# Kernel optimization log

Measured on AMD Instinct MI355X. Metric: run time of the kernel, lower is better.

Reference implementation:

```python
import jax, jax.numpy as jnp
import numpy as np

N_VEH = 40000
N_PATH = 400000
N_ACTOR = 128
N_MAP = 128
ACT_C = 32
PAT_C = 32
SIZE = N_ACTOR + N_MAP + ACT_C + PAT_C  # 320
HID = SIZE // 2  # 160
EPS = 1e-5


def _gn1(x, w, b):
    # GroupNorm with 1 group over channel dim of [N, C]: per-row normalize, per-channel affine
    mu = jnp.mean(x, axis=-1, keepdims=True)
    var = jnp.mean(jnp.square(x - mu), axis=-1, keepdims=True)
    return (x - mu) * jax.lax.rsqrt(var + EPS) * w + b


def setup_inputs() -> dict:
    key = jax.random.key(0)
    ks = jax.random.split(key, 12)
    inp = {
        "actors": jax.random.normal(ks[0], (N_VEH, N_ACTOR), jnp.float32),
        "paths": jax.random.normal(ks[1], (N_PATH, N_MAP), jnp.float32),
        "Z_act": jax.random.normal(ks[2], (N_VEH, ACT_C), jnp.float32),
        "Z_pat": jax.random.normal(ks[3], (N_PATH, PAT_C), jnp.float32),
        "u": jax.random.randint(ks[4], (N_PATH,), 0, N_VEH, jnp.int64 if jax.config.jax_enable_x64 else jnp.int32),
        # LinRes params (LaneGCN LinearRes: Linear(bias=False) -> GN -> ReLU -> Linear(bias=False) -> GN -> +transform(x) -> ReLU)
        "w1": jax.random.normal(ks[5], (HID, SIZE), jnp.float32) / np.sqrt(SIZE),
        "w2": jax.random.normal(ks[6], (HID, HID), jnp.float32) / np.sqrt(HID),
        "wt": jax.random.normal(ks[7], (HID, SIZE), jnp.float32) / np.sqrt(SIZE),
        "g1w": jnp.ones((HID,), jnp.float32),
        "g1b": jnp.zeros((HID,), jnp.float32),
        "g2w": jnp.ones((HID,), jnp.float32),
        "g2b": jnp.zeros((HID,), jnp.float32),
        # final head Linear(HID, 1)
        "wh": jax.random.normal(ks[8], (1, HID), jnp.float32) / np.sqrt(HID),
        "bh": jnp.zeros((1,), jnp.float32),
    }
    return inp


def reference(actors, paths, Z_act, Z_pat, u, w1, w2, wt, g1w, g1b, g2w, g2b, wh, bh):
    # edge-indexed gather + concat: [N_PATH, SIZE]
    x = jnp.concatenate([paths, Z_pat, actors[u], Z_act[u]], axis=-1)
    h = jnp.einsum('ns,hs->nh', x, w1)
    h = jax.nn.relu(_gn1(h, g1w, g1b))
    h = jnp.einsum('nh,gh->ng', h, w2)
    h = _gn1(h, g2w, g2b)
    h = jax.nn.relu(h + jnp.einsum('ns,hs->nh', x, wt))
    logits = jnp.einsum('nh,oh->no', h, wh) + bh
    return logits
```

## Files before the change

### kernel.cpp

```cpp
#include <hip/hip_runtime.h>
#include <hip/hip_bf16.h>

typedef short short8 __attribute__((ext_vector_type(8)));
typedef float floatx4 __attribute__((ext_vector_type(4)));

#define XP 328
#define HP 168

__device__ __forceinline__ unsigned short f2bf(float f) {
    __hip_bfloat16 h = __float2bfloat16(f);
    return __builtin_bit_cast(unsigned short, h);
}
__device__ __forceinline__ float bf2f(unsigned short s) {
    __hip_bfloat16 h = __builtin_bit_cast(__hip_bfloat16, s);
    return __bfloat162float(h);
}

__global__ void pack_wc(const float* __restrict__ w1, const float* __restrict__ wt,
                        unsigned short* __restrict__ dst) {
    int i = blockIdx.x * 256 + threadIdx.x;
    if (i >= 320 * 320) return;
    int j = i & 7;
    int lane = (i >> 3) & 63;
    int r = i >> 9;
    int kb = r % 10;
    int t = r / 10;
    int n = t * 16 + (lane & 15);
    int k = kb * 32 + ((lane >> 4) << 3) + j;
    float v = (n < 160) ? w1[n * 320 + k] : wt[(n - 160) * 320 + k];
    dst[i] = f2bf(v);
}

__global__ void pack_w2(const float* __restrict__ w2, unsigned short* __restrict__ dst) {
    int i = blockIdx.x * 256 + threadIdx.x;
    if (i >= 160 * 160) return;
    int j = i & 7;
    int lane = (i >> 3) & 63;
    int r = i >> 9;
    int kb = r % 5;
    int t = r / 5;
    int n = t * 16 + (lane & 15);
    int k = kb * 32 + ((lane >> 4) << 3) + j;
    dst[i] = f2bf(w2[n * 160 + k]);
}

__global__ __launch_bounds__(256, 3) void fused_kernel(
    const float* __restrict__ actors, const float* __restrict__ paths,
    const float* __restrict__ Z_act, const float* __restrict__ Z_pat,
    const int* __restrict__ u,
    const unsigned short* __restrict__ pB1, const unsigned short* __restrict__ pB2,
    const float* __restrict__ g1w, const float* __restrict__ g1b,
    const float* __restrict__ g2w, const float* __restrict__ g2b,
    const float* __restrict__ wh, const float* __restrict__ bh,
    float* __restrict__ out)
{
    __shared__ __align__(16) char smem[43520];
    unsigned short* lX  = (unsigned short*)smem;
    unsigned short* lH1 = (unsigned short*)smem;
    unsigned short* lHT = (unsigned short*)(smem + 21504);
    float* sSum  = (float*)(smem + 41984);
    float* sSq   = sSum + 128;
    float* sMu   = sSum + 256;
    float* sRstd = sSum + 320;

    const int tid  = threadIdx.x;
    const int wave = tid >> 6;
    const int lane = tid & 63;
    const int quad = lane >> 4;
    const int l15  = lane & 15;
    const int row0 = blockIdx.x * 64;

    float4 vD[10], vG[10];
    int uv[10];
    #pragma unroll
    for (int i = 0; i < 10; i++) {
        int f = i * 256 + tid;
        int r = f / 40, q = f - r * 40;
        const float* src = (q < 32) ? (paths + (size_t)(row0 + r) * 128 + q * 4)
                                    : (Z_pat + (size_t)(row0 + r) * 32 + (q - 32) * 4);
        vD[i] = *(const float4*)src;
        uv[i] = u[row0 + r];
    }
    #pragma unroll
    for (int i = 0; i < 10; i++) {
        int f = i * 256 + tid;
        int r = f / 40, q = f - r * 40;
        (void)r;
        int un = uv[i];
        const float* src = (q < 32) ? (actors + (size_t)un * 128 + q * 4)
                                    : (Z_act + (size_t)un * 32 + (q - 32) * 4);
        vG[i] = *(const float4*)src;
    }
    #pragma unroll
    for (int i = 0; i < 10; i++) {
        int f = i * 256 + tid;
        int r = f / 40, q = f - r * 40;
        ushort4 sv;
        sv.x = f2bf(vD[i].x); sv.y = f2bf(vD[i].y); sv.z = f2bf(vD[i].z); sv.w = f2bf(vD[i].w);
        *(ushort4*)(lX + r * XP + q * 4) = sv;
    }
    #pragma unroll
    for (int i = 0; i < 10; i++) {
        int f = i * 256 + tid;
        int r = f / 40, q = f - r * 40;
        ushort4 sv;
        sv.x = f2bf(vG[i].x); sv.y = f2bf(vG[i].y); sv.z = f2bf(vG[i].z); sv.w = f2bf(vG[i].w);
        *(ushort4*)(lX + r * XP + 160 + q * 4) = sv;
    }

    short8 bA[5], bB[5];
    #pragma unroll
    for (int ti = 0; ti < 5; ti++) {
        int t = wave * 5 + ti;
        bA[ti] = *(const short8*)(pB1 + ((size_t)(t * 10 + 0) * 64 + lane) * 8);
        bB[ti] = *(const short8*)(pB1 + ((size_t)(t * 10 + 1) * 64 + lane) * 8);
    }
    __syncthreads();

    floatx4 fzero = {0.f, 0.f, 0.f, 0.f};
    floatx4 acc[4][5];
    #pragma unroll
    for (int i = 0; i < 4; i++)
        #pragma unroll
        for (int j = 0; j < 5; j++) acc[i][j] = fzero;

    #pragma unroll
    for (int kb = 0; kb < 10; kb++) {
        short8 a[4];
        #pragma unroll
        for (int mt = 0; mt < 4; mt++)
            a[mt] = *(const short8*)(lX + (mt * 16 + l15) * XP + kb * 32 + quad * 8);
        short8 bN[5];
        if (kb + 2 < 10) {
            #pragma unroll
            for (int ti = 0; ti < 5; ti++) {
                int t = wave * 5 + ti;
                bN[ti] = *(const short8*)(pB1 + ((size_t)(t * 10 + kb + 2) * 64 + lane) * 8);
            }
        }
        #pragma unroll
        for (int ti = 0; ti < 5; ti++) {
            #pragma unroll
            for (int mt = 0; mt < 4; mt++)
                acc[mt][ti] = __builtin_amdgcn_mfma_f32_16x16x32_bf16(a[mt], bA[ti], acc[mt][ti], 0, 0, 0);
        }
        #pragma unroll
        for (int ti = 0; ti < 5; ti++) { bA[ti] = bB[ti]; bB[ti] = bN[ti]; }
    }
    __syncthreads();

    if (wave >= 2) {
        int wn = wave - 2;
        #pragma unroll
        for (int mtp = 0; mtp < 4; mtp++)
            #pragma unroll
            for (int ti = 0; ti < 5; ti++)
                #pragma unroll
                for (int r = 0; r < 4; r++)
                    lHT[((((wn * 4 + mtp) * 5 + ti) * 4 + r) << 6) + lane] = f2bf(acc[mtp][ti][r]);
    } else {
        float s[16], q2[16];
        #pragma unroll
        for (int mt = 0; mt < 4; mt++)
            #pragma unroll
            for (int r = 0; r < 4; r++) {
                float sv = 0.f, qv = 0.f;
                #pragma unroll
                for (int ti = 0; ti < 5; ti++) {
                    float v = acc[mt][ti][r];
                    sv += v; qv += v * v;
                }
                s[mt * 4 + r] = sv; q2[mt * 4 + r] = qv;
            }
        #pragma unroll
        for (int off = 1; off <= 8; off <<= 1)
            #pragma unroll
            for (int k = 0; k < 16; k++) {
                s[k]  += __shfl_xor(s[k],  off, 64);
                q2[k] += __shfl_xor(q2[k], off, 64);
            }
        if (l15 == 0) {
            #pragma unroll
            for (int mt = 0; mt < 4; mt++)
                #pragma unroll
                for (int r = 0; r < 4; r++) {
                    int m = mt * 16 + quad * 4 + r;
                    sSum[wave * 64 + m] = s[mt * 4 + r];
                    sSq[wave * 64 + m]  = q2[mt * 4 + r];
                }
        }
    }
    __syncthreads();

    if (tid < 64) {
        float ts = sSum[tid] + sSum[64 + tid];
        float tq = sSq[tid] + sSq[64 + tid];
        float mu = ts * (1.f / 160.f);
        float var = tq * (1.f / 160.f) - mu * mu;
        sMu[tid] = mu;
        sRstd[tid] = rsqrtf(var + 1e-5f);
    }
    __syncthreads();

    if (wave < 2) {
        float gw[5], gb[5];
        #pragma unroll
        for (int ti = 0; ti < 5; ti++) {
            int n = wave * 80 + ti * 16 + l15;
            gw[ti] = g1w[n]; gb[ti] = g1b[n];
        }
        #pragma unroll
        for (int mt = 0; mt < 4; mt++)
            #pragma unroll
            for (int r = 0; r < 4; r++) {
                int m = mt * 16 + quad * 4 + r;
                float mu = sMu[m], rs = sRstd[m];
                #pragma unroll
                for (int ti = 0; ti < 5; ti++) {
                    float v = (acc[mt][ti][r] - mu) * rs * gw[ti] + gb[ti];
                    v = fmaxf(v, 0.f);
                    lH1[m * HP + wave * 80 + ti * 16 + l15] = f2bf(v);
                }
            }
    }

    const int wm = wave & 1, wn = wave >> 1;
    short8 b2A[5], b2B[5];
    #pragma unroll
    for (int ti = 0; ti < 5; ti++) {
        int t = wn * 5 + ti;
        b2A[ti] = *(const short8*)(pB2 + ((size_t)(t * 5 + 0) * 64 + lane) * 8);
        b2B[ti] = *(const short8*)(pB2 + ((size_t)(t * 5 + 1) * 64 + lane) * 8);
    }
    __syncthreads();

    floatx4 acc2[2][5];
    #pragma unroll
    for (int i = 0; i < 2; i++)
        #pragma unroll
        for (int j = 0; j < 5; j++) acc2[i][j] = fzero;

    #pragma unroll
    for (int kb = 0; kb < 5; kb++) {
        short8 a[2];
        #pragma unroll
        for (int mt = 0; mt < 2; mt++)
            a[mt] = *(const short8*)(lH1 + (wm * 32 + mt * 16 + l15) * HP + kb * 32 + quad * 8);
        short8 bN[5];
        if (kb + 2 < 5) {
            #pragma unroll
            for (int ti = 0; ti < 5; ti++) {
                int t = wn * 5 + ti;
                bN[ti] = *(const short8*)(pB2 + ((size_t)(t * 5 + kb + 2) * 64 + lane) * 8);
            }
        }
        #pragma unroll
        for (int ti = 0; ti < 5; ti++) {
            #pragma unroll
            for (int mt = 0; mt < 2; mt++)
                acc2[mt][ti] = __builtin_amdgcn_mfma_f32_16x16x32_bf16(a[mt], b2A[ti], acc2[mt][ti], 0, 0, 0);
        }
        #pragma unroll
        for (int ti = 0; ti < 5; ti++) { b2A[ti] = b2B[ti]; b2B[ti] = bN[ti]; }
    }

    {
        float s[8], q2[8];
        #pragma unroll
        for (int mt = 0; mt < 2; mt++)
            #pragma unroll
            for (int r = 0; r < 4; r++) {
                float sv = 0.f, qv = 0.f;
                #pragma unroll
                for (int ti = 0; ti < 5; ti++) {
                    float v = acc2[mt][ti][r];
                    sv += v; qv += v * v;
                }
                s[mt * 4 + r] = sv; q2[mt * 4 + r] = qv;
            }
        #pragma unroll
        for (int off = 1; off <= 8; off <<= 1)
            #pragma unroll
            for (int k = 0; k < 8; k++) {
                s[k]  += __shfl_xor(s[k],  off, 64);
                q2[k] += __shfl_xor(q2[k], off, 64);
            }
        if (l15 == 0) {
            #pragma unroll
            for (int mt = 0; mt < 2; mt++)
                #pragma unroll
                for (int r = 0; r < 4; r++) {
                    int m = wm * 32 + mt * 16 + quad * 4 + r;
                    sSum[wn * 64 + m] = s[mt * 4 + r];
                    sSq[wn * 64 + m]  = q2[mt * 4 + r];
                }
        }
    }
    __syncthreads();

    if (tid < 64) {
        float ts = sSum[tid] + sSum[64 + tid];
        float tq = sSq[tid] + sSq[64 + tid];
        float mu = ts * (1.f / 160.f);
        float var = tq * (1.f / 160.f) - mu * mu;
        sMu[tid] = mu;
        sRstd[tid] = rsqrtf(var + 1e-5f);
    }
    __syncthreads();

    {
        float g2wv[5], g2bv[5], whv[5];
        #pragma unroll
        for (int ti = 0; ti < 5; ti++) {
            int n = wn * 80 + ti * 16 + l15;
            g2wv[ti] = g2w[n]; g2bv[ti] = g2b[n]; whv[ti] = wh[n];
        }
        float dp[8];
        #pragma unroll
        for (int k = 0; k < 8; k++) dp[k] = 0.f;
        #pragma unroll
        for (int mt = 0; mt < 2; mt++)
            #pragma unroll
            for (int r = 0; r < 4; r++) {
                int m = wm * 32 + mt * 16 + quad * 4 + r;
                float mu = sMu[m], rs = sRstd[m];
                #pragma unroll
                for (int ti = 0; ti < 5; ti++) {
                    float v = (acc2[mt][ti][r] - mu) * rs * g2wv[ti] + g2bv[ti];
                    v += bf2f(lHT[((((wn * 4 + (wm * 2 + mt)) * 5 + ti) * 4 + r) << 6) + lane]);
                    v = fmaxf(v, 0.f);
                    dp[mt * 4 + r] += v * whv[ti];
                }
            }
        #pragma unroll
        for (int off = 1; off <= 8; off <<= 1)
            #pragma unroll
            for (int k = 0; k < 8; k++) dp[k] += __shfl_xor(dp[k], off, 64);
        __syncthreads();
        if (l15 == 0) {
            #pragma unroll
            for (int mt = 0; mt < 2; mt++)
                #pragma unroll
                for (int r = 0; r < 4; r++) {
                    int m = wm * 32 + mt * 16 + quad * 4 + r;
                    sSum[wn * 64 + m] = dp[mt * 4 + r];
                }
        }
    }
    __syncthreads();
    if (tid < 64) out[row0 + tid] = sSum[tid] + sSum[64 + tid] + bh[0];
}

extern "C" void kernel_launch(void* const* d_in, const int* in_sizes, int n_in,
                              void* d_out, int out_size, void* d_ws, size_t ws_size,
                              hipStream_t stream) {
    const float* actors = (const float*)d_in[0];
    const float* paths  = (const float*)d_in[1];
    const float* Z_act  = (const float*)d_in[2];
    const float* Z_pat  = (const float*)d_in[3];
    const int*   u      = (const int*)d_in[4];
    const float* w1     = (const float*)d_in[5];
    const float* w2     = (const float*)d_in[6];
    const float* wt     = (const float*)d_in[7];
    const float* g1w    = (const float*)d_in[8];
    const float* g1b    = (const float*)d_in[9];
    const float* g2w    = (const float*)d_in[10];
    const float* g2b    = (const float*)d_in[11];
    const float* wh     = (const float*)d_in[12];
    const float* bh     = (const float*)d_in[13];
    float* out = (float*)d_out;

    unsigned short* pB1 = (unsigned short*)d_ws;
    unsigned short* pB2 = pB1 + 320 * 320;

    hipLaunchKernelGGL(pack_wc, dim3(400), dim3(256), 0, stream, w1, wt, pB1);
    hipLaunchKernelGGL(pack_w2, dim3(100), dim3(256), 0, stream, w2, pB2);
    hipLaunchKernelGGL(fused_kernel, dim3(400000 / 64), dim3(256), 0, stream,
                       actors, paths, Z_act, Z_pat, u, pB1, pB2,
                       g1w, g1b, g2w, g2b, wh, bh, out);
}
```

Baseline: 500.2 us.

## Shrink blocks to 32 rows and two waves, remove cross-wave GroupNorm reductions

The fused kernel now processes 32 rows per block with 128 threads, so each wave owns full 160-wide output rows in GEMM1 (wave 0 the main branch, wave 1 the transform branch) and 16 full rows in GEMM2. Row statistics for both GroupNorms are computed in-wave via shuffles, which removes the shared sSum/sSq exchange buffers and several __syncthreads barriers, and halves LDS per block. B-fragment prefetch depth goes from two steps to one with more tiles per wave. The trade-off is more blocks, higher per-thread register pressure (20 accumulators, 10-entry B buffers), and a GEMM1 split where wave 0 also does the GN1 epilogue while wave 1 only stores, so the work is imbalanced.

```diff
diff --git a/kernel.cpp b/kernel.cpp
--- a/kernel.cpp
+++ b/kernel.cpp
@@ -44,7 +44,7 @@
     dst[i] = f2bf(w2[n * 160 + k]);
 }
 
-__global__ __launch_bounds__(256, 3) void fused_kernel(
+__global__ __launch_bounds__(128, 3) void fused_kernel(
     const float* __restrict__ actors, const float* __restrict__ paths,
     const float* __restrict__ Z_act, const float* __restrict__ Z_pat,
     const int* __restrict__ u,
@@ -54,27 +54,23 @@
     const float* __restrict__ wh, const float* __restrict__ bh,
     float* __restrict__ out)
 {
-    __shared__ __align__(16) char smem[43520];
+    __shared__ __align__(16) char smem[21504];
     unsigned short* lX  = (unsigned short*)smem;
     unsigned short* lH1 = (unsigned short*)smem;
-    unsigned short* lHT = (unsigned short*)(smem + 21504);
-    float* sSum  = (float*)(smem + 41984);
-    float* sSq   = sSum + 128;
-    float* sMu   = sSum + 256;
-    float* sRstd = sSum + 320;
+    unsigned short* lHT = (unsigned short*)(smem + 10752);
 
     const int tid  = threadIdx.x;
     const int wave = tid >> 6;
     const int lane = tid & 63;
     const int quad = lane >> 4;
     const int l15  = lane & 15;
-    const int row0 = blockIdx.x * 64;
+    const int row0 = blockIdx.x * 32;
 
     float4 vD[10], vG[10];
     int uv[10];
     #pragma unroll
     for (int i = 0; i < 10; i++) {
-        int f = i * 256 + tid;
+        int f = i * 128 + tid;
         int r = f / 40, q = f - r * 40;
         const float* src = (q < 32) ? (paths + (size_t)(row0 + r) * 128 + q * 4)
                                     : (Z_pat + (size_t)(row0 + r) * 32 + (q - 32) * 4);
@@ -83,9 +79,8 @@
     }
     #pragma unroll
     for (int i = 0; i < 10; i++) {
-        int f = i * 256 + tid;
-        int r = f / 40, q = f - r * 40;
-        (void)r;
+        int f = i * 128 + tid;
+        int q = f % 40;
         int un = uv[i];
         const float* src = (q < 32) ? (actors + (size_t)un * 128 + q * 4)
                                     : (Z_act + (size_t)un * 32 + (q - 32) * 4);
@@ -93,7 +88,7 @@
     }
     #pragma unroll
     for (int i = 0; i < 10; i++) {
-        int f = i * 256 + tid;
+        int f = i * 128 + tid;
         int r = f / 40, q = f - r * 40;
         ushort4 sv;
         sv.x = f2bf(vD[i].x); sv.y = f2bf(vD[i].y); sv.z = f2bf(vD[i].z); sv.w = f2bf(vD[i].w);
@@ -101,72 +96,60 @@
     }
     #pragma unroll
     for (int i = 0; i < 10; i++) {
-        int f = i * 256 + tid;
+        int f = i * 128 + tid;
         int r = f / 40, q = f - r * 40;
         ushort4 sv;
         sv.x = f2bf(vG[i].x); sv.y = f2bf(vG[i].y); sv.z = f2bf(vG[i].z); sv.w = f2bf(vG[i].w);
         *(ushort4*)(lX + r * XP + 160 + q * 4) = sv;
     }
 
-    short8 bA[5], bB[5];
-    #pragma unroll
-    for (int ti = 0; ti < 5; ti++) {
-        int t = wave * 5 + ti;
-        bA[ti] = *(const short8*)(pB1 + ((size_t)(t * 10 + 0) * 64 + lane) * 8);
-        bB[ti] = *(const short8*)(pB1 + ((size_t)(t * 10 + 1) * 64 + lane) * 8);
+    short8 bC[10], bN[10];
+    #pragma unroll
+    for (int ti = 0; ti < 10; ti++) {
+        int t = wave * 10 + ti;
+        bC[ti] = *(const short8*)(pB1 + ((size_t)(t * 10 + 0) * 64 + lane) * 8);
     }
     __syncthreads();
 
     floatx4 fzero = {0.f, 0.f, 0.f, 0.f};
-    floatx4 acc[4][5];
-    #pragma unroll
-    for (int i = 0; i < 4; i++)
-        #pragma unroll
-        for (int j = 0; j < 5; j++) acc[i][j] = fzero;
+    floatx4 acc[2][10];
+    #pragma unroll
+    for (int i = 0; i < 2; i++)
+        #pragma unroll
+        for (int j = 0; j < 10; j++) acc[i][j] = fzero;
 
     #pragma unroll
     for (int kb = 0; kb < 10; kb++) {
-        short8 a[4];
-        #pragma unroll
-        for (int mt = 0; mt < 4; mt++)
+        short8 a[2];
+        #pragma unroll
+        for (int mt = 0; mt < 2; mt++)
             a[mt] = *(const short8*)(lX + (mt * 16 + l15) * XP + kb * 32 + quad * 8);
-        short8 bN[5];
-        if (kb + 2 < 10) {
-            #pragma unroll
-            for (int ti = 0; ti < 5; ti++) {
-                int t = wave * 5 + ti;
-                bN[ti] = *(const short8*)(pB1 + ((size_t)(t * 10 + kb + 2) * 64 + lane) * 8);
-            }
-        }
-        #pragma unroll
-        for (int ti = 0; ti < 5; ti++) {
-            #pragma unroll
-            for (int mt = 0; mt < 4; mt++)
-                acc[mt][ti] = __builtin_amdgcn_mfma_f32_16x16x32_bf16(a[mt], bA[ti], acc[mt][ti], 0, 0, 0);
-        }
-        #pragma unroll
-        for (int ti = 0; ti < 5; ti++) { bA[ti] = bB[ti]; bB[ti] = bN[ti]; }
+        if (kb < 9) {
+            #pragma unroll
+            for (int ti = 0; ti < 10; ti++) {
+                int t = wave * 10 + ti;
+                bN[ti] = *(const short8*)(pB1 + ((size_t)(t * 10 + kb + 1) * 64 + lane) * 8);
+            }
+        }
+        #pragma unroll
+        for (int ti = 0; ti < 10; ti++)
+            #pragma unroll
+            for (int mt = 0; mt < 2; mt++)
+                acc[mt][ti] = __builtin_amdgcn_mfma_f32_16x16x32_bf16(a[mt], bC[ti], acc[mt][ti], 0, 0, 0);
+        #pragma unroll
+        for (int ti = 0; ti < 10; ti++) bC[ti] = bN[ti];
     }
     __syncthreads();
 
-    if (wave >= 2) {
-        int wn = wave - 2;
-        #pragma unroll
-        for (int mtp = 0; mtp < 4; mtp++)
-            #pragma unroll
-            for (int ti = 0; ti < 5; ti++)
-                #pragma unroll
-                for (int r = 0; r < 4; r++)
-                    lHT[((((wn * 4 + mtp) * 5 + ti) * 4 + r) << 6) + lane] = f2bf(acc[mtp][ti][r]);
-    } else {
-        float s[16], q2[16];
-        #pragma unroll
-        for (int mt = 0; mt < 4; mt++)
+    if (wave == 0) {
+        float s[8], q2[8];
+        #pragma unroll
+        for (int mt = 0; mt < 2; mt++)
             #pragma unroll
             for (int r = 0; r < 4; r++) {
                 float sv = 0.f, qv = 0.f;
                 #pragma unroll
-                for (int ti = 0; ti < 5; ti++) {
+                for (int ti = 0; ti < 10; ti++) {
                     float v = acc[mt][ti][r];
                     sv += v; qv += v * v;
                 }
@@ -175,180 +158,121 @@
         #pragma unroll
         for (int off = 1; off <= 8; off <<= 1)
             #pragma unroll
-            for (int k = 0; k < 16; k++) {
+            for (int k = 0; k < 8; k++) {
                 s[k]  += __shfl_xor(s[k],  off, 64);
                 q2[k] += __shfl_xor(q2[k], off, 64);
             }
-        if (l15 == 0) {
-            #pragma unroll
-            for (int mt = 0; mt < 4; mt++)
+        float gw[10], gb[10];
+        #pragma unroll
+        for (int ti = 0; ti < 10; ti++) {
+            int n = ti * 16 + l15;
+            gw[ti] = g1w[n]; gb[ti] = g1b[n];
+        }
+        #pragma unroll
+        for (int mt = 0; mt < 2; mt++)
+            #pragma unroll
+            for (int r = 0; r < 4; r++) {
+                float mu = s[mt * 4 + r] * (1.f / 160.f);
+                float var = q2[mt * 4 + r] * (1.f / 160.f) - mu * mu;
+                float rs = rsqrtf(var + 1e-5f);
+                int m = mt * 16 + quad * 4 + r;
+                #pragma unroll
+                for (int ti = 0; ti < 10; ti++) {
+                    float v = (acc[mt][ti][r] - mu) * rs * gw[ti] + gb[ti];
+                    v = fmaxf(v, 0.f);
+                    lH1[m * HP + ti * 16 + l15] = f2bf(v);
+                }
+            }
+    } else {
+        #pragma unroll
+        for (int mt = 0; mt < 2; mt++)
+            #pragma unroll
+            for (int ti = 0; ti < 10; ti++)
                 #pragma unroll
                 for (int r = 0; r < 4; r++) {
                     int m = mt * 16 + quad * 4 + r;
-                    sSum[wave * 64 + m] = s[mt * 4 + r];
-                    sSq[wave * 64 + m]  = q2[mt * 4 + r];
+                    lHT[m * HP + ti * 16 + l15] = f2bf(acc[mt][ti][r]);
                 }
-        }
-    }
+    }
+
+    short8 b2C[10], b2N[10];
+    #pragma unroll
+    for (int ti = 0; ti < 10; ti++)
+        b2C[ti] = *(const short8*)(pB2 + ((size_t)(ti * 5 + 0) * 64 + lane) * 8);
     __syncthreads();
 
-    if (tid < 64) {
-        float ts = sSum[tid] + sSum[64 + tid];
-        float tq = sSq[tid] + sSq[64 + tid];
-        float mu = ts * (1.f / 160.f);
-        float var = tq * (1.f / 160.f) - mu * mu;
-        sMu[tid] = mu;
-        sRstd[tid] = rsqrtf(var + 1e-5f);
-    }
-    __syncthreads();
-
-    if (wave < 2) {
-        float gw[5], gb[5];
-        #pragma unroll
-        for (int ti = 0; ti < 5; ti++) {
-            int n = wave * 80 + ti * 16 + l15;
-            gw[ti] = g1w[n]; gb[ti] = g1b[n];
-        }
-        #pragma unroll
-        for (int mt = 0; mt < 4; mt++)
+    floatx4 acc2[10];
+    #pragma unroll
+    for (int j = 0; j < 10; j++) acc2[j] = fzero;
+
+    #pragma unroll
+    for (int kb = 0; kb < 5; kb++) {
+        short8 a = *(const short8*)(lH1 + (wave * 16 + l15) * HP + kb * 32 + quad * 8);
+        if (kb < 4) {
+            #pragma unroll
+            for (int ti = 0; ti < 10; ti++)
+                b2N[ti] = *(const short8*)(pB2 + ((size_t)(ti * 5 + kb + 1) * 64 + lane) * 8);
+        }
+        #pragma unroll
+        for (int ti = 0; ti < 10; ti++)
+            acc2[ti] = __builtin_amdgcn_mfma_f32_16x16x32_bf16(a, b2C[ti], acc2[ti], 0, 0, 0);
+        #pragma unroll
+        for (int ti = 0; ti < 10; ti++) b2C[ti] = b2N[ti];
+    }
+
+    {
+        float s[4], q2[4];
+        #pragma unroll
+        for (int r = 0; r < 4; r++) {
+            float sv = 0.f, qv = 0.f;
+            #pragma unroll
+            for (int ti = 0; ti < 10; ti++) {
+                float v = acc2[ti][r];
+                sv += v; qv += v * v;
+            }
+            s[r] = sv; q2[r] = qv;
+        }
+        #pragma unroll
+        for (int off = 1; off <= 8; off <<= 1)
             #pragma unroll
             for (int r = 0; r < 4; r++) {
-                int m = mt * 16 + quad * 4 + r;
-                float mu = sMu[m], rs = sRstd[m];
-                #pragma unroll
-                for (int ti = 0; ti < 5; ti++) {
-                    float v = (acc[mt][ti][r] - mu) * rs * gw[ti] + gb[ti];
-                    v = fmaxf(v, 0.f);
-                    lH1[m * HP + wave * 80 + ti * 16 + l15] = f2bf(v);
-                }
-            }
-    }
-
-    const int wm = wave & 1, wn = wave >> 1;
-    short8 b2A[5], b2B[5];
-    #pragma unroll
-    for (int ti = 0; ti < 5; ti++) {
-        int t = wn * 5 + ti;
-        b2A[ti] = *(const short8*)(pB2 + ((size_t)(t * 5 + 0) * 64 + lane) * 8);
-        b2B[ti] = *(const short8*)(pB2 + ((size_t)(t * 5 + 1) * 64 + lane) * 8);
-    }
-    __syncthreads();
-
-    floatx4 acc2[2][5];
-    #pragma unroll
-    for (int i = 0; i < 2; i++)
-        #pragma unroll
-        for (int j = 0; j < 5; j++) acc2[i][j] = fzero;
-
-    #pragma unroll
-    for (int kb = 0; kb < 5; kb++) {
-        short8 a[2];
-        #pragma unroll
-        for (int mt = 0; mt < 2; mt++)
-            a[mt] = *(const short8*)(lH1 + (wm * 32 + mt * 16 + l15) * HP + kb * 32 + quad * 8);
-        short8 bN[5];
-        if (kb + 2 < 5) {
-            #pragma unroll
-            for (int ti = 0; ti < 5; ti++) {
-                int t = wn * 5 + ti;
-                bN[ti] = *(const short8*)(pB2 + ((size_t)(t * 5 + kb + 2) * 64 + lane) * 8);
-            }
-        }
-        #pragma unroll
-        for (int ti = 0; ti < 5; ti++) {
-            #pragma unroll
-            for (int mt = 0; mt < 2; mt++)
-                acc2[mt][ti] = __builtin_amdgcn_mfma_f32_16x16x32_bf16(a[mt], b2A[ti], acc2[mt][ti], 0, 0, 0);
-        }
-        #pragma unroll
-        for (int ti = 0; ti < 5; ti++) { b2A[ti] = b2B[ti]; b2B[ti] = bN[ti]; }
-    }
-
-    {
-        float s[8], q2[8];
-        #pragma unroll
-        for (int mt = 0; mt < 2; mt++)
-            #pragma unroll
-            for (int r = 0; r < 4; r++) {
-                float sv = 0.f, qv = 0.f;
-                #pragma unroll
-                for (int ti = 0; ti < 5; ti++) {
-                    float v = acc2[mt][ti][r];
-                    sv += v; qv += v * v;
-                }
-                s[mt * 4 + r] = sv; q2[mt * 4 + r] = qv;
-            }
+                s[r]  += __shfl_xor(s[r],  off, 64);
+                q2[r] += __shfl_xor(q2[r], off, 64);
+            }
+        float g2wv[10], g2bv[10], whv[10];
+        #pragma unroll
+        for (int ti = 0; ti < 10; ti++) {
+            int n = ti * 16 + l15;
+            g2wv[ti] = g2w[n]; g2bv[ti] = g2b[n]; whv[ti] = wh[n];
+        }
+        float dp[4];
+        #pragma unroll
+        for (int r = 0; r < 4; r++) {
+            float mu = s[r] * (1.f / 160.f);
+            float var = q2[r] * (1.f / 160.f) - mu * mu;
+            float rs = rsqrtf(var + 1e-5f);
+            int m = wave * 16 + quad * 4 + r;
+            float d = 0.f;
+            #pragma unroll
+            for (int ti = 0; ti < 10; ti++) {
+                float v = (acc2[ti][r] - mu) * rs * g2wv[ti] + g2bv[ti];
+                v += bf2f(lHT[m * HP + ti * 16 + l15]);
+                v = fmaxf(v, 0.f);
+                d += v * whv[ti];
+            }
+            dp[r] = d;
+        }
         #pragma unroll
         for (int off = 1; off <= 8; off <<= 1)
             #pragma unroll
-            for (int k = 0; k < 8; k++) {
-                s[k]  += __shfl_xor(s[k],  off, 64);
-                q2[k] += __shfl_xor(q2[k], off, 64);
-            }
+            for (int r = 0; r < 4; r++) dp[r] += __shfl_xor(dp[r], off, 64);
         if (l15 == 0) {
-            #pragma unroll
-            for (int mt = 0; mt < 2; mt++)
-                #pragma unroll
-                for (int r = 0; r < 4; r++) {
-                    int m = wm * 32 + mt * 16 + quad * 4 + r;
-                    sSum[wn * 64 + m] = s[mt * 4 + r];
-                    sSq[wn * 64 + m]  = q2[mt * 4 + r];
-                }
-        }
-    }
-    __syncthreads();
-
-    if (tid < 64) {
-        float ts = sSum[tid] + sSum[64 + tid];
-        float tq = sSq[tid] + sSq[64 + tid];
-        float mu = ts * (1.f / 160.f);
-        float var = tq * (1.f / 160.f) - mu * mu;
-        sMu[tid] = mu;
-        sRstd[tid] = rsqrtf(var + 1e-5f);
-    }
-    __syncthreads();
-
-    {
-        float g2wv[5], g2bv[5], whv[5];
-        #pragma unroll
-        for (int ti = 0; ti < 5; ti++) {
-            int n = wn * 80 + ti * 16 + l15;
-            g2wv[ti] = g2w[n]; g2bv[ti] = g2b[n]; whv[ti] = wh[n];
-        }
-        float dp[8];
-        #pragma unroll
-        for (int k = 0; k < 8; k++) dp[k] = 0.f;
-        #pragma unroll
-        for (int mt = 0; mt < 2; mt++)
-            #pragma unroll
-            for (int r = 0; r < 4; r++) {
-                int m = wm * 32 + mt * 16 + quad * 4 + r;
-                float mu = sMu[m], rs = sRstd[m];
-                #pragma unroll
-                for (int ti = 0; ti < 5; ti++) {
-                    float v = (acc2[mt][ti][r] - mu) * rs * g2wv[ti] + g2bv[ti];
-                    v += bf2f(lHT[((((wn * 4 + (wm * 2 + mt)) * 5 + ti) * 4 + r) << 6) + lane]);
-                    v = fmaxf(v, 0.f);
-                    dp[mt * 4 + r] += v * whv[ti];
-                }
-            }
-        #pragma unroll
-        for (int off = 1; off <= 8; off <<= 1)
-            #pragma unroll
-            for (int k = 0; k < 8; k++) dp[k] += __shfl_xor(dp[k], off, 64);
-        __syncthreads();
-        if (l15 == 0) {
-            #pragma unroll
-            for (int mt = 0; mt < 2; mt++)
-                #pragma unroll
-                for (int r = 0; r < 4; r++) {
-                    int m = wm * 32 + mt * 16 + quad * 4 + r;
-                    sSum[wn * 64 + m] = dp[mt * 4 + r];
-                }
-        }
-    }
-    __syncthreads();
-    if (tid < 64) out[row0 + tid] = sSum[tid] + sSum[64 + tid] + bh[0];
+            float bh0 = bh[0];
+            #pragma unroll
+            for (int r = 0; r < 4; r++)
+                out[row0 + wave * 16 + quad * 4 + r] = dp[r] + bh0;
+        }
+    }
 }
 
 extern "C" void kernel_launch(void* const* d_in, const int* in_sizes, int n_in,
@@ -375,7 +299,7 @@
 
     hipLaunchKernelGGL(pack_wc, dim3(400), dim3(256), 0, stream, w1, wt, pB1);
     hipLaunchKernelGGL(pack_w2, dim3(100), dim3(256), 0, stream, w2, pB2);
-    hipLaunchKernelGGL(fused_kernel, dim3(400000 / 64), dim3(256), 0, stream,
+    hipLaunchKernelGGL(fused_kernel, dim3(400000 / 32), dim3(128), 0, stream,
                        actors, paths, Z_act, Z_pat, u, pB1, pB2,
                        g1w, g1b, g2w, g2b, wh, bh, out);
 }
```

Result: slower. 568.2 us (+13.6%).
